# Kernel tuning notes

Measured on AMD Instinct MI355X. Metric: run time of the kernel, lower is better.

## Reference

```python
import jax, jax.numpy as jnp
import numpy as np

N_NODES = 20000
N_EDGES = 320000
C = 64  # classes
NEG_SLOPE = 0.2  # DGL GATConv default


def setup_inputs() -> dict:
    key = jax.random.key(0)
    ks = jax.random.split(key, 32)
    dims = [C, 2 * C, 4 * C, 8 * C, 16 * C]
    inp = {}
    inp["feat"] = jax.random.normal(ks[0], (N_NODES, C), jnp.float32)
    k = 1
    for i in range(4):
        din, dout = dims[i], dims[i + 1]
        scale = 1.0 / np.sqrt(din)
        inp[f"W{i+1}"] = jax.random.normal(ks[k], (din, dout), jnp.float32) * scale; k += 1
        inp[f"al{i+1}"] = jax.random.normal(ks[k], (dout,), jnp.float32) * 0.1; k += 1
        inp[f"ar{i+1}"] = jax.random.normal(ks[k], (dout,), jnp.float32) * 0.1; k += 1
        inp[f"b{i+1}"] = jnp.zeros((dout,), jnp.float32)
    inp["relW"] = jax.random.normal(ks[k], (16 * C, C), jnp.float32) * (1.0 / np.sqrt(16 * C)); k += 1
    inp["relB"] = jnp.zeros((C,), jnp.float32)
    inp["src"] = jax.random.randint(ks[k], (N_EDGES,), 0, N_NODES, jnp.int32); k += 1
    inp["dst"] = jax.random.randint(ks[k], (N_EDGES,), 0, N_NODES, jnp.int32); k += 1
    inp["rel"] = jnp.ones((C,), jnp.int32)
    inp["order"] = 1023
    return inp


def _gat_layer(x, W, al, ar, b, src, dst, n_nodes):
    """DGL GATConv (num_heads=1, allow_zero_in_degree=True, activation=tanh)."""
    h = x @ W                                   # [N, D] projected features
    el = h @ al                                 # [N] attn_l score per node
    er = h @ ar                                 # [N] attn_r score per node
    e = jax.nn.leaky_relu(el[src] + er[dst], NEG_SLOPE)          # [E]
    # segment (edge) softmax over incoming edges of each dst node
    m = jax.ops.segment_max(e, dst, num_segments=n_nodes)        # [N]
    ex = jnp.exp(e - m[dst])                                      # [E]
    s = jax.ops.segment_sum(ex, dst, num_segments=n_nodes)       # [N]
    alpha = ex / s[dst]                                           # [E]
    # gather neighbor messages, weight by attention, scatter-add to dst
    out = jax.ops.segment_sum(h[src] * alpha[:, None], dst, num_segments=n_nodes)  # [N, D]
    return jnp.tanh(out + b)


def reference(feat, W1, al1, ar1, b1, W2, al2, ar2, b2, W3, al3, ar3, b3,
              W4, al4, ar4, b4, relW, relB, src, dst, rel, order):
    n = feat.shape[0]
    h = _gat_layer(feat, W1, al1, ar1, b1, src, dst, n)
    h = _gat_layer(h, W2, al2, ar2, b2, src, dst, n)
    h = _gat_layer(h, W3, al3, ar3, b3, src, dst, n)
    h = _gat_layer(h, W4, al4, ar4, b4, src, dst, n)
    embeddings = h[: order + 1]                  # first order+1 node embeddings
    pooling = jnp.mean(embeddings, axis=0)       # [16C]
    logits = pooling @ relW + relB               # [C]
    nz = jnp.nonzero(rel, size=rel.shape[0])[0]  # static-size nonzero (rel is all-ones)
    return logits[nz]
```

## Files before the change

kernel.cpp:

```cpp
#include <hip/hip_runtime.h>
#include <hip/hip_bf16.h>

#define NN 20000
#define NE 320000
#define MPAD 20096
#define ORD 1024
#define NB 79

typedef __hip_bfloat16 bf16;
typedef __attribute__((ext_vector_type(8))) short bf16x8;
typedef __attribute__((ext_vector_type(4))) float f32x4;

static __device__ __forceinline__ float b2f(bf16 x) { return __bfloat162float(x); }
static __device__ __forceinline__ float bfbits2f(short s) {
    unsigned int u = ((unsigned int)(unsigned short)s) << 16;
    float f; __builtin_memcpy(&f, &u, 4); return f;
}
static __device__ __forceinline__ short f2bfbits(float v) {
    bf16 h = __float2bfloat16(v);
    short s; __builtin_memcpy(&s, &h, 2); return s;
}
static __device__ __forceinline__ unsigned short f2bfu(float v) {
    bf16 h = __float2bfloat16(v);
    unsigned short s; __builtin_memcpy(&s, &h, 2); return s;
}

__global__ void setup_all(const float* __restrict__ feat,
                          const float* __restrict__ W1, const float* __restrict__ al1, const float* __restrict__ ar1,
                          const float* __restrict__ W2, const float* __restrict__ al2, const float* __restrict__ ar2,
                          const float* __restrict__ W3, const float* __restrict__ al3, const float* __restrict__ ar3,
                          const float* __restrict__ W4, const float* __restrict__ al4, const float* __restrict__ ar4,
                          bf16* __restrict__ featb, bf16* __restrict__ wt1,
                          bf16* __restrict__ wt2, bf16* __restrict__ wt3,
                          bf16* __restrict__ wt4, int* __restrict__ counts,
                          int* __restrict__ hglob,
                          float* __restrict__ walbuf, float* __restrict__ warbuf) {
    int b = blockIdx.x;
    if (b < 960) {
        const float *W, *al, *ar; int dout, k; float *wal, *war;
        if (b < 64)       { W = W1; al = al1; ar = ar1; dout = 128;  k = b;       wal = walbuf;        war = warbuf; }
        else if (b < 192) { W = W2; al = al2; ar = ar2; dout = 256;  k = b - 64;  wal = walbuf + 512;  war = warbuf + 512; }
        else if (b < 448) { W = W3; al = al3; ar = ar3; dout = 512;  k = b - 192; wal = walbuf + 1024; war = warbuf + 1024; }
        else              { W = W4; al = al4; ar = ar4; dout = 1024; k = b - 448; wal = walbuf + 1536; war = warbuf + 1536; }
        const float* row = W + (long)k * dout;
        float sl = 0.f, sr = 0.f;
        for (int j = threadIdx.x; j < dout; j += 256) {
            float w = row[j];
            sl += w * al[j];
            sr += w * ar[j];
        }
        __shared__ float sbl[256], sbr[256];
        sbl[threadIdx.x] = sl; sbr[threadIdx.x] = sr;
        __syncthreads();
        for (int st = 128; st > 0; st >>= 1) {
            if (threadIdx.x < st) {
                sbl[threadIdx.x] += sbl[threadIdx.x + st];
                sbr[threadIdx.x] += sbr[threadIdx.x + st];
            }
            __syncthreads();
        }
        if (threadIdx.x == 0) { wal[k] = sbl[0]; war[k] = sbr[0]; }
        return;
    }
    int i = (b - 960) * 256 + threadIdx.x;
    if (i < NN) counts[i] = 0;
    if (i < 256) hglob[i] = 0;
    if (i < 1280000) { featb[i] = __float2bfloat16(feat[i]); return; }
    i -= 1280000;
    if (i < 8192)  { int r = i >> 7,  c = i & 127;  wt1[c * 64 + r]  = __float2bfloat16(W1[i]); return; }
    i -= 8192;
    if (i < 32768) { int r = i >> 8,  c = i & 255;  wt2[c * 128 + r] = __float2bfloat16(W2[i]); return; }
    i -= 32768;
    if (i < 131072){ int r = i >> 9,  c = i & 511;  wt3[c * 256 + r] = __float2bfloat16(W3[i]); return; }
    i -= 131072;
    if (i < 524288){ int r = i >> 10, c = i & 1023; wt4[c * 512 + r] = __float2bfloat16(W4[i]); return; }
}

__global__ void hist_kernel(const int* __restrict__ dst, int* __restrict__ counts, int n) {
    int i = blockIdx.x * blockDim.x + threadIdx.x;
    if (i < n) atomicAdd(&counts[dst[i]], 1);
}

__global__ void csr_phase1(const int* __restrict__ counts, int* __restrict__ blocksums,
                           int* __restrict__ hglob) {
    __shared__ int sb[256];
    __shared__ int hh[256];
    int tid = threadIdx.x;
    hh[tid] = 0;
    int i = blockIdx.x * 256 + tid;
    int c = (i < NN) ? counts[i] : 0;
    sb[tid] = c;
    __syncthreads();
    for (int st = 128; st > 0; st >>= 1) {
        if (tid < st) sb[tid] += sb[tid + st];
        __syncthreads();
    }
    if (tid == 0) blocksums[blockIdx.x] = sb[0];
    if (i < NN) {
        int d = c > 255 ? 255 : c;
        atomicAdd(&hh[d], 1);
    }
    __syncthreads();
    if (hh[tid] > 0) atomicAdd(&hglob[tid], hh[tid]);
}

__global__ void csr_phase2(const int* __restrict__ counts, const int* __restrict__ blocksums,
                           int* __restrict__ offsets, int* __restrict__ cursor,
                           const int* __restrict__ hglob, int* __restrict__ curg) {
    int tid = threadIdx.x;
    if (blockIdx.x == NB) {
        __shared__ int hs[256];
        int orig = hglob[tid];
        hs[tid] = orig;
        __syncthreads();
        for (int st = 1; st < 256; st <<= 1) {
            int u = (tid >= st) ? hs[tid - st] : 0;
            __syncthreads();
            hs[tid] += u;
            __syncthreads();
        }
        curg[tid] = hs[tid] - orig;
        return;
    }
    __shared__ int bs[256];
    bs[tid] = (tid < NB) ? blocksums[tid] : 0;
    __syncthreads();
    for (int st = 1; st < 256; st <<= 1) {
        int u = (tid >= st) ? bs[tid - st] : 0;
        __syncthreads();
        bs[tid] += u;
        __syncthreads();
    }
    int base = (blockIdx.x == 0) ? 0 : bs[blockIdx.x - 1];
    __shared__ int sc[256];
    int i = blockIdx.x * 256 + tid;
    int c = (i < NN) ? counts[i] : 0;
    sc[tid] = c;
    __syncthreads();
    for (int st = 1; st < 256; st <<= 1) {
        int u = (tid >= st) ? sc[tid - st] : 0;
        __syncthreads();
        sc[tid] += u;
        __syncthreads();
    }
    int excl = base + sc[tid] - c;
    if (i < NN) { offsets[i] = excl; cursor[i] = excl; }
    if (i == NN - 1) offsets[NN] = excl + c;
}

__global__ void scatter_elr(const int* __restrict__ src, const int* __restrict__ dst,
                            int* __restrict__ cursor, int* __restrict__ esrc,
                            const int* __restrict__ counts, int* __restrict__ curg,
                            int* __restrict__ nodeperm,
                            const bf16* __restrict__ X, const float* __restrict__ wal,
                            const float* __restrict__ war, float* __restrict__ el,
                            float* __restrict__ er) {
    int b = blockIdx.x;
    if (b < 1250) {
        int i = b * 256 + threadIdx.x;
        int p = atomicAdd(&cursor[dst[i]], 1);
        esrc[p] = src[i];
        return;
    }
    if (b < 1250 + NB) {
        __shared__ int hh[256];
        __shared__ int basep[256];
        int tid = threadIdx.x;
        hh[tid] = 0;
        __syncthreads();
        int i = (b - 1250) * 256 + tid;
        int d = 0, rank = 0;
        bool valid = (i < NN);
        if (valid) {
            d = counts[i]; if (d > 255) d = 255;
            rank = atomicAdd(&hh[d], 1);
        }
        __syncthreads();
        if (hh[tid] > 0) basep[tid] = atomicAdd(&curg[tid], hh[tid]);
        __syncthreads();
        if (valid) nodeperm[basep[d] + rank] = i;
        return;
    }
    int idx = (b - 1250 - NB) * 256 + threadIdx.x;
    int node = idx >> 6;
    int lane = threadIdx.x & 63;
    if (node >= NN) return;
    float x = bfbits2f(*((const short*)X + (long)node * 64 + lane));
    float sl = x * wal[lane];
    float sr = x * war[lane];
    #pragma unroll
    for (int o = 32; o > 0; o >>= 1) {
        sl += __shfl_down(sl, o);
        sr += __shfl_down(sr, o);
    }
    if (lane == 0) { el[node] = sl; er[node] = sr; }
}

__global__ void aggregate_sm(const bf16* __restrict__ X,
                             const float* __restrict__ el, const float* __restrict__ er,
                             const int* __restrict__ esrc, const int* __restrict__ off,
                             const int* __restrict__ perm, float* __restrict__ zbuf, int zn,
                             bf16* __restrict__ Y, int din, int log2chunks, int nmax) {
    __shared__ __attribute__((aligned(16))) float alds[32][68];
    {
        int z = blockIdx.x * 256 + threadIdx.x;
        if (z < zn) zbuf[z] = 0.f;
    }
    int chunk = blockIdx.x & ((1 << log2chunks) - 1);
    int nb = blockIdx.x >> log2chunks;
    int sub = threadIdx.x >> 3, sl = threadIdx.x & 7;
    int slot = nb * 32 + sub;
    if (slot >= nmax) return;
    int node = perm ? perm[slot] : slot;
    int s = off[node], e = off[node + 1];
    int deg = e - s;
    bool fast = (deg <= 64);

    float erd = (deg > 0) ? er[node] : 0.f;
    float vmax = -1e30f, inv = 0.f;
    if (fast) {
        float v[8];
        #pragma unroll
        for (int t = 0; t < 8; t++) {
            v[t] = -1e30f;
            int idx = sl + 8 * t;
            if (idx < deg) {
                float x = el[esrc[s + idx]] + erd;
                v[t] = x >= 0.f ? x : 0.2f * x;
            }
            vmax = fmaxf(vmax, v[t]);
        }
        #pragma unroll
        for (int o = 1; o < 8; o <<= 1) vmax = fmaxf(vmax, __shfl_xor(vmax, o));
        float ssum = 0.f;
        #pragma unroll
        for (int t = 0; t < 8; t++) {
            int idx = sl + 8 * t;
            if (idx < deg) { v[t] = __expf(v[t] - vmax); ssum += v[t]; }
        }
        #pragma unroll
        for (int o = 1; o < 8; o <<= 1) ssum += __shfl_xor(ssum, o);
        inv = 1.f / ssum;
        #pragma unroll
        for (int t = 0; t < 8; t++) {
            int idx = sl + 8 * t;
            if (idx < deg) alds[sub][idx] = v[t] * inv;
        }
    } else {
        for (int j = s + sl; j < e; j += 8) {
            float x = el[esrc[j]] + erd;
            x = x >= 0.f ? x : 0.2f * x;
            vmax = fmaxf(vmax, x);
        }
        #pragma unroll
        for (int o = 1; o < 8; o <<= 1) vmax = fmaxf(vmax, __shfl_xor(vmax, o));
        float ssum = 0.f;
        for (int j = s + sl; j < e; j += 8) {
            float x = el[esrc[j]] + erd;
            x = x >= 0.f ? x : 0.2f * x;
            ssum += __expf(x - vmax);
        }
        #pragma unroll
        for (int o = 1; o < 8; o <<= 1) ssum += __shfl_xor(ssum, o);
        inv = 1.f / ssum;
    }

    const short* xb = (const short*)X + chunk * 64 + sl * 8;
    float acc[8] = {0.f,0.f,0.f,0.f,0.f,0.f,0.f,0.f};
    int j = s;
    if (fast) {
        for (; j + 8 <= e; j += 8) {
            int ofs = j - s;
            f32x4 a0 = *(const f32x4*)&alds[sub][ofs];
            f32x4 a1 = *(const f32x4*)&alds[sub][ofs + 4];
            int r[8]; bf16x8 w[8];
            #pragma unroll
            for (int q = 0; q < 8; q++) r[q] = esrc[j + q];
            #pragma unroll
            for (int q = 0; q < 8; q++) w[q] = *(const bf16x8*)(xb + (long)r[q] * din);
            #pragma unroll
            for (int q = 0; q < 4; q++)
                #pragma unroll
                for (int v = 0; v < 8; v++) acc[v] += a0[q] * bfbits2f(w[q][v]);
            #pragma unroll
            for (int q = 0; q < 4; q++)
                #pragma unroll
                for (int v = 0; v < 8; v++) acc[v] += a1[q] * bfbits2f(w[4 + q][v]);
        }
        for (; j + 4 <= e; j += 4) {
            int ofs = j - s;
            f32x4 a0 = *(const f32x4*)&alds[sub][ofs];
            int r[4]; bf16x8 w[4];
            #pragma unroll
            for (int q = 0; q < 4; q++) r[q] = esrc[j + q];
            #pragma unroll
            for (int q = 0; q < 4; q++) w[q] = *(const bf16x8*)(xb + (long)r[q] * din);
            #pragma unroll
            for (int q = 0; q < 4; q++)
                #pragma unroll
                for (int v = 0; v < 8; v++) acc[v] += a0[q] * bfbits2f(w[q][v]);
        }
        for (; j < e; j++) {
            float a = alds[sub][j - s];
            bf16x8 w = *(const bf16x8*)(xb + (long)esrc[j] * din);
            #pragma unroll
            for (int v = 0; v < 8; v++) acc[v] += a * bfbits2f(w[v]);
        }
    } else {
        for (; j + 8 <= e; j += 8) {
            int r[8]; float a[8]; bf16x8 w[8];
            #pragma unroll
            for (int q = 0; q < 8; q++) r[q] = esrc[j + q];
            #pragma unroll
            for (int q = 0; q < 8; q++) {
                float x = el[r[q]] + erd;
                x = x >= 0.f ? x : 0.2f * x;
                a[q] = __expf(x - vmax) * inv;
            }
            #pragma unroll
            for (int q = 0; q < 8; q++) w[q] = *(const bf16x8*)(xb + (long)r[q] * din);
            #pragma unroll
            for (int q = 0; q < 8; q++)
                #pragma unroll
                for (int v = 0; v < 8; v++) acc[v] += a[q] * bfbits2f(w[q][v]);
        }
        for (; j < e; j++) {
            int r = esrc[j];
            float x = el[r] + erd;
            x = x >= 0.f ? x : 0.2f * x;
            float a = __expf(x - vmax) * inv;
            bf16x8 w = *(const bf16x8*)(xb + (long)r * din);
            #pragma unroll
            for (int v = 0; v < 8; v++) acc[v] += a * bfbits2f(w[v]);
        }
    }
    short outv[8];
    #pragma unroll
    for (int v = 0; v < 8; v++) outv[v] = f2bfbits(acc[v]);
    bf16x8 store;
    __builtin_memcpy(&store, outv, sizeof(store));
    *(bf16x8*)((short*)Y + (long)node * din + chunk * 64 + sl * 8) = store;
}

__global__ __launch_bounds__(256, 4)
void gemm_k64(const bf16* __restrict__ A, const bf16* __restrict__ WT,
              const float* __restrict__ bias, bf16* __restrict__ C,
              const float* __restrict__ wal, const float* __restrict__ war,
              float* __restrict__ elp, float* __restrict__ erp) {
    int gw = blockIdx.x * 4 + (threadIdx.x >> 6);
    if (gw >= 2500) return;
    int r0 = (gw >> 1) << 4;
    int col0 = (gw & 1) << 6;
    int lane = threadIdx.x & 63;
    int m = lane & 15, quad = lane >> 4;

    const short* Ab = (const short*)A + (long)(r0 + m) * 64 + quad * 8;
    bf16x8 a0 = *(const bf16x8*)(Ab);
    bf16x8 a1 = *(const bf16x8*)(Ab + 32);

    f32x4 acc[4];
    bf16x8 b0[4], b1[4];
    #pragma unroll
    for (int t = 0; t < 4; t++) {
        acc[t] = (f32x4){0.f, 0.f, 0.f, 0.f};
        const short* Bb = (const short*)WT + (long)(col0 + t * 16 + m) * 64 + quad * 8;
        b0[t] = *(const bf16x8*)(Bb);
        b1[t] = *(const bf16x8*)(Bb + 32);
    }
    #pragma unroll
    for (int t = 0; t < 4; t++) {
        acc[t] = __builtin_amdgcn_mfma_f32_16x16x32_bf16(a0, b0[t], acc[t], 0, 0, 0);
        acc[t] = __builtin_amdgcn_mfma_f32_16x16x32_bf16(a1, b1[t], acc[t], 0, 0, 0);
    }

    float sl4[4] = {0.f, 0.f, 0.f, 0.f};
    float sr4[4] = {0.f, 0.f, 0.f, 0.f};
    #pragma unroll
    for (int t = 0; t < 4; t++) {
        int col = col0 + t * 16 + m;
        float bb = bias[col];
        float wl = wal[col], wrr = war[col];
        #pragma unroll
        for (int r = 0; r < 4; r++) {
            float v = tanhf(acc[t][r] + bb);
            sl4[r] += v * wl;
            sr4[r] += v * wrr;
            float vn = __shfl_xor(v, 1);
            if ((m & 1) == 0) {
                unsigned int pk = (unsigned int)f2bfu(v) | ((unsigned int)f2bfu(vn) << 16);
                int row = r0 + quad * 4 + r;
                *(unsigned int*)((short*)C + (long)row * 128 + col) = pk;
            }
        }
    }
    #pragma unroll
    for (int r = 0; r < 4; r++) {
        float s1 = sl4[r], s2 = sr4[r];
        #pragma unroll
        for (int o = 1; o < 16; o <<= 1) {
            s1 += __shfl_xor(s1, o);
            s2 += __shfl_xor(s2, o);
        }
        if (m == 0) {
            int row = r0 + quad * 4 + r;
            atomicAdd(&elp[row], s1);
            atomicAdd(&erp[row], s2);
        }
    }
}

__global__ __launch_bounds__(256, 4)
void gemm_tiled(const bf16* __restrict__ A, const bf16* __restrict__ WT,
                const float* __restrict__ bias, bf16* __restrict__ C,
                const float* __restrict__ wal, const float* __restrict__ war,
                float* __restrict__ elp, float* __restrict__ erp,
                float* __restrict__ poolacc,
                int M, int K, int N, int ncols, int nrows) {
    __shared__ short smem[16384];
    short* As = smem;
    short* Bs = smem + 8192;
    int g = blockIdx.x;
    int rowTile = ((g >> 3) / ncols) * 8 + (g & 7);
    int colTile = (g >> 3) % ncols;
    if (rowTile >= nrows) return;
    int row0 = rowTile << 7, col0 = colTile << 7;
    int tid = threadIdx.x;
    int lane = tid & 63, wave = tid >> 6;
    int wr = (wave >> 1) << 6;
    int wc = (wave & 1) << 6;
    int m = lane & 15, quad = lane >> 4;

    f32x4 acc[4][4];
    #pragma unroll
    for (int i = 0; i < 4; i++)
        #pragma unroll
        for (int j = 0; j < 4; j++) acc[i][j] = (f32x4){0.f, 0.f, 0.f, 0.f};

    const short* Ab = (const short*)A;
    const short* Bb = (const short*)WT;
    long ga[4], gb[4];
    #pragma unroll
    for (int n = 0; n < 4; n++) {
        int chunk = n * 256 + tid;
        int row = chunk >> 3;
        int qg = (chunk & 7) ^ (row & 7);
        ga[n] = (long)(row0 + row) * K + qg * 8;
        gb[n] = (long)(col0 + row) * K + qg * 8;
    }

    typedef const __attribute__((address_space(1))) void cgvoid;
    typedef __attribute__((address_space(3))) void lvoid;

    for (int k0 = 0; k0 < K; k0 += 64) {
        __syncthreads();
        #pragma unroll
        for (int n = 0; n < 4; n++)
            __builtin_amdgcn_global_load_lds((cgvoid*)(Ab + ga[n] + k0),
                                             (lvoid*)(As + (n * 256 + tid) * 8), 16, 0, 0);
        #pragma unroll
        for (int n = 0; n < 4; n++)
            __builtin_amdgcn_global_load_lds((cgvoid*)(Bb + gb[n] + k0),
                                             (lvoid*)(Bs + (n * 256 + tid) * 8), 16, 0, 0);
        __syncthreads();
        #pragma unroll
        for (int h = 0; h < 2; h++) {
            bf16x8 af[4], bfr[4];
            #pragma unroll
            for (int s = 0; s < 4; s++) {
                int ra = wr + s * 16 + m;
                int sa = (h * 4 + quad) ^ (ra & 7);
                af[s] = *(const bf16x8*)(As + ra * 64 + sa * 8);
                int rb = wc + s * 16 + m;
                int sb = (h * 4 + quad) ^ (rb & 7);
                bfr[s] = *(const bf16x8*)(Bs + rb * 64 + sb * 8);
            }
            #pragma unroll
            for (int i = 0; i < 4; i++)
                #pragma unroll
                for (int j = 0; j < 4; j++)
                    acc[i][j] = __builtin_amdgcn_mfma_f32_16x16x32_bf16(af[i], bfr[j], acc[i][j], 0, 0, 0);
        }
    }

    float bb[4], walr[4], warr[4];
    #pragma unroll
    for (int j = 0; j < 4; j++) {
        int col = col0 + wc + j * 16 + m;
        bb[j] = bias[col];
        if (elp) { walr[j] = wal[col]; warr[j] = war[col]; }
    }
    float colsum[4] = {0.f, 0.f, 0.f, 0.f};
    __syncthreads();
    short* myep = smem + wave * 1152;
    #pragma unroll
    for (int i = 0; i < 4; i++) {
        float sl4[4] = {0.f, 0.f, 0.f, 0.f};
        float sr4[4] = {0.f, 0.f, 0.f, 0.f};
        #pragma unroll
        for (int j = 0; j < 4; j++) {
            #pragma unroll
            for (int r = 0; r < 4; r++) {
                float v = tanhf(acc[i][j][r] + bb[j]);
                if (elp) { sl4[r] += v * walr[j]; sr4[r] += v * warr[j]; }
                if (poolacc) colsum[j] += v;
                float vn = __shfl_xor(v, 1);
                if ((m & 1) == 0) {
                    unsigned int pk = (unsigned int)f2bfu(v) | ((unsigned int)f2bfu(vn) << 16);
                    *(unsigned int*)(myep + (quad * 4 + r) * 72 + j * 16 + m) = pk;
                }
            }
        }
        #pragma unroll
        for (int pass = 0; pass < 2; pass++) {
            int lr = pass * 8 + (lane >> 3);
            int lc = (lane & 7) * 8;
            bf16x8 v = *(const bf16x8*)(myep + lr * 72 + lc);
            int row = row0 + wr + i * 16 + lr;
            if (row < M)
                *(bf16x8*)((short*)C + (long)row * N + col0 + wc + lc) = v;
        }
        if (elp) {
            #pragma unroll
            for (int r = 0; r < 4; r++) {
                float s1 = sl4[r], s2 = sr4[r];
                #pragma unroll
                for (int o = 1; o < 16; o <<= 1) {
                    s1 += __shfl_xor(s1, o);
                    s2 += __shfl_xor(s2, o);
                }
                if (m == 0) {
                    int row = row0 + wr + i * 16 + quad * 4 + r;
                    if (row < M) {
                        atomicAdd(&elp[row], s1);
                        atomicAdd(&erp[row], s2);
                    }
                }
            }
        }
    }
    if (poolacc) {
        #pragma unroll
        for (int j = 0; j < 4; j++) {
            float cs = colsum[j];
            cs += __shfl_xor(cs, 16);
            cs += __shfl_xor(cs, 32);
            if (quad == 0)
                atomicAdd(&poolacc[col0 + wc + j * 16 + m], cs);
        }
    }
}

__global__ void head_small(const float* __restrict__ poolsum, const float* __restrict__ relW,
                           const float* __restrict__ relB, const int* __restrict__ order,
                           const int* __restrict__ rel, float* __restrict__ out) {
    __shared__ float ps[1024];
    __shared__ float part[4][64];
    int tid = threadIdx.x;
    for (int i = tid; i < 1024; i += 256) ps[i] = poolsum[i];
    __syncthreads();
    int t = tid & 63, p = tid >> 6;
    const float* wp = relW + (long)p * 256 * 64 + t;
    float s = 0.f;
    #pragma unroll 8
    for (int c = 0; c < 256; c++) s += ps[p * 256 + c] * wp[(long)c * 64];
    part[p][t] = s;
    __syncthreads();
    if (tid < 64) {
        float rows = (float)(order[0] + 1);
        float lv = (part[0][tid] + part[1][tid] + part[2][tid] + part[3][tid]) / rows + relB[tid];
        int rv = rel[tid];
        unsigned long long mask = __ballot(rv != 0);
        int pos = __popcll(mask & ((1ULL << tid) - 1));
        int count = __popcll(mask);
        float l0 = __shfl(lv, 0);
        if (rv) out[pos] = lv;
        if (tid >= count) out[tid] = l0;
    }
}

extern "C" void kernel_launch(void* const* d_in, const int* in_sizes, int n_in,
                              void* d_out, int out_size, void* d_ws, size_t ws_size,
                              hipStream_t stream) {
    const float* feat = (const float*)d_in[0];
    const float* W[4]  = {(const float*)d_in[1], (const float*)d_in[5], (const float*)d_in[9],  (const float*)d_in[13]};
    const float* al[4] = {(const float*)d_in[2], (const float*)d_in[6], (const float*)d_in[10], (const float*)d_in[14]};
    const float* ar[4] = {(const float*)d_in[3], (const float*)d_in[7], (const float*)d_in[11], (const float*)d_in[15]};
    const float* bias[4] = {(const float*)d_in[4], (const float*)d_in[8], (const float*)d_in[12], (const float*)d_in[16]};
    const float* relW = (const float*)d_in[17];
    const float* relB = (const float*)d_in[18];
    const int* src = (const int*)d_in[19];
    const int* dst = (const int*)d_in[20];
    const int* rel = (const int*)d_in[21];
    const int* order = (const int*)d_in[22];

    const int dims[5] = {64, 128, 256, 512, 1024};

    char* p = (char*)d_ws;
    auto carve = [&](size_t bytes) {
        void* r = (void*)p;
        p += (bytes + 255) & ~(size_t)255;
        return r;
    };
    bf16* xbuf = (bf16*)carve((size_t)MPAD * 1024 * sizeof(bf16));
    bf16* ybuf = (bf16*)carve((size_t)MPAD * 512 * sizeof(bf16));
    bf16* featb = (bf16*)carve((size_t)MPAD * 64 * sizeof(bf16));
    bf16* wt[4];
    for (int l = 0; l < 4; l++)
        wt[l] = (bf16*)carve((size_t)dims[l] * dims[l + 1] * sizeof(bf16));
    float* walbuf = (float*)carve(4 * 512 * sizeof(float));
    float* warbuf = (float*)carve(4 * 512 * sizeof(float));
    float* elbuf[2];
    elbuf[0] = (float*)carve((size_t)2 * NN * sizeof(float));
    elbuf[1] = (float*)carve((size_t)2 * NN * sizeof(float));
    int* counts  = (int*)carve((size_t)NN * sizeof(int));
    int* offsets = (int*)carve((size_t)(NN + 1) * sizeof(int));
    int* cursor  = (int*)carve((size_t)NN * sizeof(int));
    int* esrc    = (int*)carve((size_t)NE * sizeof(int));
    int* nodeperm = (int*)carve((size_t)NN * sizeof(int));
    int* blocksums = (int*)carve((size_t)NB * sizeof(int));
    int* hglob   = (int*)carve(256 * sizeof(int));
    int* curg    = (int*)carve(256 * sizeof(int));
    float* poolsum = (float*)carve(1024 * sizeof(float));

    setup_all<<<960 + 7720, 256, 0, stream>>>(
        feat, W[0], al[0], ar[0], W[1], al[1], ar[1],
        W[2], al[2], ar[2], W[3], al[3], ar[3],
        featb, wt[0], wt[1], wt[2], wt[3], counts, hglob, walbuf, warbuf);

    hist_kernel<<<(NE + 255) / 256, 256, 0, stream>>>(dst, counts, NE);
    csr_phase1<<<NB, 256, 0, stream>>>(counts, blocksums, hglob);
    csr_phase2<<<NB + 1, 256, 0, stream>>>(counts, blocksums, offsets, cursor, hglob, curg);
    scatter_elr<<<1250 + NB + 5000, 256, 0, stream>>>(src, dst, cursor, esrc,
                                                      counts, curg, nodeperm,
                                                      featb, walbuf, warbuf,
                                                      elbuf[0], elbuf[0] + NN);

    const bf16* x = featb;
    const int nrows = MPAD / 128;
    const int nrowsPad = 160;
    const int log2c[4] = {0, 1, 2, 3};
    for (int l = 0; l < 4; l++) {
        int K = dims[l], N = dims[l + 1];
        float* elr_rd = elbuf[l & 1];
        float* elr_wr = elbuf[(l + 1) & 1];
        int nmax  = (l < 3) ? NN : ORD;
        int nodeBlocks = (nmax + 31) / 32;
        const int* aggPerm = (l < 3) ? nodeperm : nullptr;
        float* zbuf = (l < 3) ? elr_wr : poolsum;
        int zn = (l < 3) ? 2 * NN : 1024;
        aggregate_sm<<<nodeBlocks << log2c[l], 256, 0, stream>>>(
            x, elr_rd, elr_rd + NN, esrc, offsets, aggPerm, zbuf, zn, ybuf, K, log2c[l], nmax);
        int ncols = N >> 7;
        if (l == 0) {
            gemm_k64<<<625, 256, 0, stream>>>(ybuf, wt[0], bias[0], xbuf,
                                              walbuf + 512, warbuf + 512,
                                              elr_wr, elr_wr + NN);
        } else if (l < 3) {
            gemm_tiled<<<nrowsPad * ncols, 256, 0, stream>>>(
                ybuf, wt[l], bias[l], xbuf,
                walbuf + (l + 1) * 512, warbuf + (l + 1) * 512,
                elr_wr, elr_wr + NN, nullptr,
                NN, K, N, ncols, nrows);
        } else {
            gemm_tiled<<<8 * ncols, 256, 0, stream>>>(
                ybuf, wt[l], bias[l], xbuf,
                nullptr, nullptr, nullptr, nullptr, poolsum,
                ORD, K, N, ncols, 8);
        }
        x = xbuf;
    }

    head_small<<<1, 256, 0, stream>>>(poolsum, relW, relB, order, rel, (float*)d_out);
}
```

Baseline: 290.6 us.

## Merge CSR build kernels via grid-wide spin sync and fold head into last GEMM

```diff
diff --git a/kernel.cpp b/kernel.cpp
--- a/kernel.cpp
+++ b/kernel.cpp
@@ -11,6 +11,8 @@
 typedef __attribute__((ext_vector_type(8))) short bf16x8;
 typedef __attribute__((ext_vector_type(4))) float f32x4;
 
+#define SCOPE_AGENT __HIP_MEMORY_SCOPE_AGENT
+
 static __device__ __forceinline__ float b2f(bf16 x) { return __bfloat162float(x); }
 static __device__ __forceinline__ float bfbits2f(short s) {
     unsigned int u = ((unsigned int)(unsigned short)s) << 16;
@@ -23,6 +25,15 @@
 static __device__ __forceinline__ unsigned short f2bfu(float v) {
     bf16 h = __float2bfloat16(v);
     unsigned short s; __builtin_memcpy(&s, &h, 2); return s;
+}
+static __device__ __forceinline__ int aload(const int* p) {
+    return __hip_atomic_load(p, __ATOMIC_RELAXED, SCOPE_AGENT);
+}
+static __device__ __forceinline__ void astore(int* p, int v) {
+    __hip_atomic_store(p, v, __ATOMIC_RELAXED, SCOPE_AGENT);
+}
+static __device__ __forceinline__ float aloadf(const float* p) {
+    return __hip_atomic_load(p, __ATOMIC_RELAXED, SCOPE_AGENT);
 }
 
 __global__ void setup_all(const float* __restrict__ feat,
@@ -33,7 +44,7 @@
                           bf16* __restrict__ featb, bf16* __restrict__ wt1,
                           bf16* __restrict__ wt2, bf16* __restrict__ wt3,
                           bf16* __restrict__ wt4, int* __restrict__ counts,
-                          int* __restrict__ hglob,
+                          int* __restrict__ hglob, int* __restrict__ syncbuf,
                           float* __restrict__ walbuf, float* __restrict__ warbuf) {
     int b = blockIdx.x;
     if (b < 960) {
@@ -64,7 +75,7 @@
     }
     int i = (b - 960) * 256 + threadIdx.x;
     if (i < NN) counts[i] = 0;
-    if (i < 256) hglob[i] = 0;
+    if (i < 256) { hglob[i] = 0; syncbuf[i] = 0; }
     if (i < 1280000) { featb[i] = __float2bfloat16(feat[i]); return; }
     i -= 1280000;
     if (i < 8192)  { int r = i >> 7,  c = i & 127;  wt1[c * 64 + r]  = __float2bfloat16(W1[i]); return; }
@@ -76,41 +87,24 @@
     if (i < 524288){ int r = i >> 10, c = i & 1023; wt4[c * 512 + r] = __float2bfloat16(W4[i]); return; }
 }
 
-__global__ void hist_kernel(const int* __restrict__ dst, int* __restrict__ counts, int n) {
-    int i = blockIdx.x * blockDim.x + threadIdx.x;
-    if (i < n) atomicAdd(&counts[dst[i]], 1);
-}
-
-__global__ void csr_phase1(const int* __restrict__ counts, int* __restrict__ blocksums,
-                           int* __restrict__ hglob) {
-    __shared__ int sb[256];
-    __shared__ int hh[256];
-    int tid = threadIdx.x;
-    hh[tid] = 0;
-    int i = blockIdx.x * 256 + tid;
-    int c = (i < NN) ? counts[i] : 0;
-    sb[tid] = c;
-    __syncthreads();
-    for (int st = 128; st > 0; st >>= 1) {
-        if (tid < st) sb[tid] += sb[tid + st];
-        __syncthreads();
-    }
-    if (tid == 0) blocksums[blockIdx.x] = sb[0];
-    if (i < NN) {
-        int d = c > 255 ? 255 : c;
-        atomicAdd(&hh[d], 1);
-    }
-    __syncthreads();
-    if (hh[tid] > 0) atomicAdd(&hglob[tid], hh[tid]);
-}
-
-__global__ void csr_phase2(const int* __restrict__ counts, const int* __restrict__ blocksums,
-                           int* __restrict__ offsets, int* __restrict__ cursor,
-                           const int* __restrict__ hglob, int* __restrict__ curg) {
-    int tid = threadIdx.x;
-    if (blockIdx.x == NB) {
-        __shared__ int hs[256];
-        int orig = hglob[tid];
+__global__ void csr_build(const int* __restrict__ dst, int* __restrict__ counts,
+                          int* __restrict__ blocksums, int* __restrict__ blockbase,
+                          int* __restrict__ hglob,
+                          int* __restrict__ offsets, int* __restrict__ cursor,
+                          int* __restrict__ curg, int* __restrict__ sync) {
+    int b = blockIdx.x, tid = threadIdx.x;
+    if (b < 1250) {
+        int i = b * 256 + tid;
+        atomicAdd(&counts[dst[i]], 1);
+        __syncthreads();
+        if (tid == 0) __hip_atomic_fetch_add(&sync[0], 1, __ATOMIC_RELEASE, SCOPE_AGENT);
+        return;
+    }
+    if (b == 1250 + NB) {
+        if (tid == 0) while (aload(&sync[1]) != NB) __builtin_amdgcn_s_sleep(8);
+        __syncthreads();
+        __shared__ int hs[256], bs[256];
+        int orig = aload(&hglob[tid]);
         hs[tid] = orig;
         __syncthreads();
         for (int st = 1; st < 256; st <<= 1) {
@@ -120,21 +114,27 @@
             __syncthreads();
         }
         curg[tid] = hs[tid] - orig;
+        int v = (tid < NB) ? aload(&blocksums[tid]) : 0;
+        bs[tid] = v;
+        __syncthreads();
+        for (int st = 1; st < 256; st <<= 1) {
+            int u = (tid >= st) ? bs[tid - st] : 0;
+            __syncthreads();
+            bs[tid] += u;
+            __syncthreads();
+        }
+        if (tid < NB) astore(&blockbase[tid], bs[tid] - v);
+        __syncthreads();
+        if (tid == 0) __hip_atomic_store(&sync[2], 1, __ATOMIC_RELEASE, SCOPE_AGENT);
         return;
     }
-    __shared__ int bs[256];
-    bs[tid] = (tid < NB) ? blocksums[tid] : 0;
+    int pb = b - 1250;
+    if (tid == 0) while (aload(&sync[0]) != 1250) __builtin_amdgcn_s_sleep(8);
     __syncthreads();
-    for (int st = 1; st < 256; st <<= 1) {
-        int u = (tid >= st) ? bs[tid - st] : 0;
-        __syncthreads();
-        bs[tid] += u;
-        __syncthreads();
-    }
-    int base = (blockIdx.x == 0) ? 0 : bs[blockIdx.x - 1];
-    __shared__ int sc[256];
-    int i = blockIdx.x * 256 + tid;
-    int c = (i < NN) ? counts[i] : 0;
+    __shared__ int sc[256], hh[256];
+    hh[tid] = 0;
+    int i = pb * 256 + tid;
+    int c = (i < NN) ? aload(&counts[i]) : 0;
     sc[tid] = c;
     __syncthreads();
     for (int st = 1; st < 256; st <<= 1) {
@@ -143,6 +143,17 @@
         sc[tid] += u;
         __syncthreads();
     }
+    if (tid == 255) astore(&blocksums[pb], sc[255]);
+    if (i < NN) { int d = c > 255 ? 255 : c; atomicAdd(&hh[d], 1); }
+    __syncthreads();
+    if (hh[tid] > 0) atomicAdd(&hglob[tid], hh[tid]);
+    __syncthreads();
+    if (tid == 0) {
+        __hip_atomic_fetch_add(&sync[1], 1, __ATOMIC_RELEASE, SCOPE_AGENT);
+        while (aload(&sync[2]) == 0) __builtin_amdgcn_s_sleep(8);
+    }
+    __syncthreads();
+    int base = aload(&blockbase[pb]);
     int excl = base + sc[tid] - c;
     if (i < NN) { offsets[i] = excl; cursor[i] = excl; }
     if (i == NN - 1) offsets[NN] = excl + c;
@@ -415,6 +426,9 @@
                 const float* __restrict__ wal, const float* __restrict__ war,
                 float* __restrict__ elp, float* __restrict__ erp,
                 float* __restrict__ poolacc,
+                const float* __restrict__ relW, const float* __restrict__ relB,
+                const int* __restrict__ order, const int* __restrict__ rel,
+                float* __restrict__ headout,
                 int M, int K, int N, int ncols, int nrows) {
     __shared__ short smem[16384];
     short* As = smem;
@@ -548,33 +562,38 @@
                 atomicAdd(&poolacc[col0 + wc + j * 16 + m], cs);
         }
     }
-}
-
-__global__ void head_small(const float* __restrict__ poolsum, const float* __restrict__ relW,
-                           const float* __restrict__ relB, const int* __restrict__ order,
-                           const int* __restrict__ rel, float* __restrict__ out) {
-    __shared__ float ps[1024];
-    __shared__ float part[4][64];
-    int tid = threadIdx.x;
-    for (int i = tid; i < 1024; i += 256) ps[i] = poolsum[i];
-    __syncthreads();
-    int t = tid & 63, p = tid >> 6;
-    const float* wp = relW + (long)p * 256 * 64 + t;
-    float s = 0.f;
-    #pragma unroll 8
-    for (int c = 0; c < 256; c++) s += ps[p * 256 + c] * wp[(long)c * 64];
-    part[p][t] = s;
-    __syncthreads();
-    if (tid < 64) {
-        float rows = (float)(order[0] + 1);
-        float lv = (part[0][tid] + part[1][tid] + part[2][tid] + part[3][tid]) / rows + relB[tid];
-        int rv = rel[tid];
-        unsigned long long mask = __ballot(rv != 0);
-        int pos = __popcll(mask & ((1ULL << tid) - 1));
-        int count = __popcll(mask);
-        float l0 = __shfl(lv, 0);
-        if (rv) out[pos] = lv;
-        if (tid >= count) out[tid] = l0;
+    if (headout) {
+        __syncthreads();
+        __shared__ int lastf;
+        if (tid == 0) {
+            unsigned int old = __hip_atomic_fetch_add((unsigned int*)&poolacc[1024], 1u,
+                                                      __ATOMIC_ACQ_REL, SCOPE_AGENT);
+            lastf = (old == 63u) ? 1 : 0;
+        }
+        __syncthreads();
+        if (!lastf) return;
+        float* ps = (float*)smem;
+        float (*part)[64] = (float(*)[64])(smem + 2048);
+        for (int i = tid; i < 1024; i += 256) ps[i] = aloadf(&poolacc[i]);
+        __syncthreads();
+        int t = tid & 63, p = tid >> 6;
+        const float* wp = relW + (long)p * 256 * 64 + t;
+        float s = 0.f;
+        #pragma unroll 8
+        for (int c = 0; c < 256; c++) s += ps[p * 256 + c] * wp[(long)c * 64];
+        part[p][t] = s;
+        __syncthreads();
+        if (tid < 64) {
+            float rows = (float)(order[0] + 1);
+            float lv = (part[0][tid] + part[1][tid] + part[2][tid] + part[3][tid]) / rows + relB[tid];
+            int rv = rel[tid];
+            unsigned long long mask = __ballot(rv != 0);
+            int pos = __popcll(mask & ((1ULL << tid) - 1));
+            int count = __popcll(mask);
+            float l0 = __shfl(lv, 0);
+            if (rv) headout[pos] = lv;
+            if (tid >= count) headout[tid] = l0;
+        }
     }
 }
 
@@ -617,19 +636,21 @@
     int* cursor  = (int*)carve((size_t)NN * sizeof(int));
     int* esrc    = (int*)carve((size_t)NE * sizeof(int));
     int* nodeperm = (int*)carve((size_t)NN * sizeof(int));
-    int* blocksums = (int*)carve((size_t)NB * sizeof(int));
+    int* blocksums = (int*)carve(128 * sizeof(int));
+    int* blockbase = (int*)carve(128 * sizeof(int));
     int* hglob   = (int*)carve(256 * sizeof(int));
     int* curg    = (int*)carve(256 * sizeof(int));
-    float* poolsum = (float*)carve(1024 * sizeof(float));
+    int* syncbuf = (int*)carve(256 * sizeof(int));
+    float* poolsum = (float*)carve(1056 * sizeof(float));
 
     setup_all<<<960 + 7720, 256, 0, stream>>>(
         feat, W[0], al[0], ar[0], W[1], al[1], ar[1],
         W[2], al[2], ar[2], W[3], al[3], ar[3],
-        featb, wt[0], wt[1], wt[2], wt[3], counts, hglob, walbuf, warbuf);
-
-    hist_kernel<<<(NE + 255) / 256, 256, 0, stream>>>(dst, counts, NE);
-    csr_phase1<<<NB, 256, 0, stream>>>(counts, blocksums, hglob);
-    csr_phase2<<<NB + 1, 256, 0, stream>>>(counts, blocksums, offsets, cursor, hglob, curg);
+        featb, wt[0], wt[1], wt[2], wt[3], counts, hglob, syncbuf, walbuf, warbuf);
+
+    csr_build<<<1250 + NB + 1, 256, 0, stream>>>(dst, counts, blocksums, blockbase,
+                                                 hglob, offsets, cursor, curg, syncbuf);
+
     scatter_elr<<<1250 + NB + 5000, 256, 0, stream>>>(src, dst, cursor, esrc,
                                                       counts, curg, nodeperm,
                                                       featb, walbuf, warbuf,
@@ -647,7 +668,7 @@
         int nodeBlocks = (nmax + 31) / 32;
         const int* aggPerm = (l < 3) ? nodeperm : nullptr;
         float* zbuf = (l < 3) ? elr_wr : poolsum;
-        int zn = (l < 3) ? 2 * NN : 1024;
+        int zn = (l < 3) ? 2 * NN : 1025;
         aggregate_sm<<<nodeBlocks << log2c[l], 256, 0, stream>>>(
             x, elr_rd, elr_rd + NN, esrc, offsets, aggPerm, zbuf, zn, ybuf, K, log2c[l], nmax);
         int ncols = N >> 7;
@@ -660,15 +681,15 @@
                 ybuf, wt[l], bias[l], xbuf,
                 walbuf + (l + 1) * 512, warbuf + (l + 1) * 512,
                 elr_wr, elr_wr + NN, nullptr,
+                nullptr, nullptr, nullptr, nullptr, nullptr,
                 NN, K, N, ncols, nrows);
         } else {
             gemm_tiled<<<8 * ncols, 256, 0, stream>>>(
                 ybuf, wt[l], bias[l], xbuf,
                 nullptr, nullptr, nullptr, nullptr, poolsum,
+                relW, relB, order, rel, (float*)d_out,
                 ORD, K, N, ncols, 8);
         }
         x = xbuf;
     }
-
-    head_small<<<1, 256, 0, stream>>>(poolsum, relW, relB, order, rel, (float*)d_out);
-}
+}
```

Result: slower. 322.5 us (+11.0%).
